# Kernel tuning notes

Hardware: AMD Instinct MI355X
Metric: run time of the kernel (lower is better)

## Reference

```python
import jax, jax.numpy as jnp
import numpy as np

N = 50000      # nodes
E = 800000     # edges (before self-loops)
F_IN = 128
F_OUT = 128
H = 4          # heads
SLOPE = 0.2    # LeakyReLU negative slope (PyG GATConv default)


def setup_inputs() -> dict:
    key = jax.random.key(0)
    ks = jax.random.split(key, 8)
    x = jax.random.normal(ks[0], (N, F_IN), dtype=jnp.float32)
    edge_index = jax.random.randint(ks[1], (2, E), 0, N, dtype=jnp.int64)
    W = jax.random.normal(ks[2], (H, F_IN, F_OUT), dtype=jnp.float32) * (1.0 / np.sqrt(F_IN))
    att_src = jax.random.normal(ks[3], (H, F_OUT), dtype=jnp.float32) * (1.0 / np.sqrt(F_OUT))
    att_dst = jax.random.normal(ks[4], (H, F_OUT), dtype=jnp.float32) * (1.0 / np.sqrt(F_OUT))
    bias = jnp.zeros((H, F_OUT), dtype=jnp.float32)
    W_out = jax.random.normal(ks[5], (H * F_OUT, F_OUT), dtype=jnp.float32) * (1.0 / np.sqrt(H * F_OUT))
    b_out = jnp.zeros((F_OUT,), dtype=jnp.float32)
    return {"x": x, "edge_index": edge_index, "W": W, "att_src": att_src,
            "att_dst": att_dst, "bias": bias, "W_out": W_out, "b_out": b_out}


def _gat_head(x, src, dst, W_h, a_src, a_dst, b_h):
    # x: [N, F_in]; src/dst: [E'] edge endpoints (messages flow src -> dst)
    xW = x @ W_h                                   # [N, F_out]
    alpha_s = xW @ a_src                           # [N]
    alpha_d = xW @ a_dst                           # [N]
    logits = alpha_s[src] + alpha_d[dst]           # [E']
    logits = jnp.where(logits > 0, logits, SLOPE * logits)  # leaky_relu
    # segment softmax over edges grouped by destination node
    seg_max = jax.ops.segment_max(logits, dst, num_segments=N)  # [N]
    e = jnp.exp(logits - seg_max[dst])             # [E']
    denom = jax.ops.segment_sum(e, dst, num_segments=N)         # [N]
    alpha = e / denom[dst]                         # [E']
    # weighted scatter-aggregate of source features to destinations
    out = jax.ops.segment_sum(alpha[:, None] * xW[src], dst, num_segments=N)  # [N, F_out]
    return out + b_h


def reference(x, edge_index, W, att_src, att_dst, bias, W_out, b_out):
    # add self-loops (PyG GATConv default)
    loops = jnp.arange(N, dtype=edge_index.dtype)
    src = jnp.concatenate([edge_index[0], loops])
    dst = jnp.concatenate([edge_index[1], loops])
    heads = [_gat_head(x, src, dst, W[h], att_src[h], att_dst[h], bias[h]) for h in range(H)]
    h_cat = jnp.concatenate(heads, axis=1)         # [N, H*F_out]
    return jax.nn.relu(h_cat @ W_out + b_out)      # [N, F_out]
```

## Files before the change

kernel.cpp:

```cpp
#include <hip/hip_runtime.h>
#include <hip/hip_bf16.h>

constexpr int NN = 50000;
constexpr int EE = 800000;
constexpr float SLOPE = 0.2f;
constexpr int NPAD = 50176;
constexpr int CAP = 64;
constexpr int ZE = NN * CAP;

typedef __bf16 bf16x8 __attribute__((ext_vector_type(8)));
typedef __bf16 bf16x4 __attribute__((ext_vector_type(4)));
typedef float f32x4 __attribute__((ext_vector_type(4)));
typedef float f32x2 __attribute__((ext_vector_type(2)));

__device__ __forceinline__ int edge_at(const int* e32, const long long* e64, int use64, long i) {
    return use64 ? (int)e64[i] : e32[i];
}

__device__ __forceinline__ f32x2 bfpair(unsigned u) {
    f32x2 r;
    r.x = __uint_as_float(u << 16);
    r.y = __uint_as_float(u & 0xffff0000u);
    return r;
}

__global__ void k_prec(const float* __restrict__ W, const float* __restrict__ Wout,
                       const float* __restrict__ att_s, const float* __restrict__ att_d,
                       const float* __restrict__ bias, const float* __restrict__ bout,
                       const long long* e64, int* flag, int* cnt,
                       __bf16* __restrict__ Bfrag, float* __restrict__ wsv, float* __restrict__ wdv,
                       float* __restrict__ cvec, uint4* __restrict__ ew) {
    int b = blockIdx.x, t = threadIdx.x;
    if (b < 512) {
        int h = b >> 7, k = b & 127;
        float acc = 0.f;
        for (int j = 0; j < 128; j++) {
            float w = W[((size_t)(h * 128 + k)) * 128 + j];
            acc += w * Wout[((size_t)(h * 128 + j)) * 128 + t];
        }
        int K = h * 128 + k;
        int k0i = K >> 5, kb = (K >> 3) & 3, jj = K & 7;
        int ni = t >> 4, lr = t & 15;
        Bfrag[(((size_t)k0i * 8 + ni) * 64 + kb * 16 + lr) * 8 + jj] = (__bf16)acc;
    } else if (b == 512) {
        float acc = bout[t];
        for (int j = 0; j < 512; j++) acc += bias[j] * Wout[(size_t)j * 128 + t];
        cvec[t] = acc;
        if (t == 0) ew[ZE] = make_uint4(0u, 0u, 0u, 0u);
    } else if (b < 517) {
        int h = b - 513;
        float as = 0.f, ad = 0.f;
        for (int j = 0; j < 128; j++) {
            float w = W[((size_t)(h * 128 + t)) * 128 + j];
            as += w * att_s[h * 128 + j];
            ad += w * att_d[h * 128 + j];
        }
        wsv[h * 128 + t] = as;
        wdv[h * 128 + t] = ad;
    } else {
        int i = (b - 517) * 128 + t;
        if (i < NN) cnt[i] = 0;
        if (b == 517 && t < 64) {
            long long v = e64[t];
            bool ok = (v >= 0) && (v < (long long)NN);
            unsigned long long m = __ballot(ok);
            if (t == 0) *flag = (m == 0xFFFFFFFFFFFFFFFFull) ? 1 : 0;
        }
    }
}

__global__ __launch_bounds__(256) void k_prep(const float* __restrict__ x, const float* __restrict__ wsv,
                                              const float* __restrict__ wdv, __bf16* __restrict__ xb,
                                              float* __restrict__ as_, float* __restrict__ ad_) {
    int n = blockIdx.x * blockDim.x + threadIdx.x;
    if (n >= NN) return;
    const float4* xr = (const float4*)(x + (size_t)n * 128);
    __bf16* xo = xb + (size_t)n * 128;
    float s[4] = {0, 0, 0, 0}, d[4] = {0, 0, 0, 0};
    for (int q = 0; q < 32; q += 2) {
        float4 v0 = xr[q], v1 = xr[q + 1];
        bf16x8 o;
        o[0] = (__bf16)v0.x; o[1] = (__bf16)v0.y; o[2] = (__bf16)v0.z; o[3] = (__bf16)v0.w;
        o[4] = (__bf16)v1.x; o[5] = (__bf16)v1.y; o[6] = (__bf16)v1.z; o[7] = (__bf16)v1.w;
        *(bf16x8*)(xo + q * 4) = o;
        #pragma unroll
        for (int h = 0; h < 4; h++) {
            float4 a0 = ((const float4*)(wsv + h * 128))[q];
            float4 a1 = ((const float4*)(wsv + h * 128))[q + 1];
            float4 b0 = ((const float4*)(wdv + h * 128))[q];
            float4 b1 = ((const float4*)(wdv + h * 128))[q + 1];
            s[h] += v0.x * a0.x + v0.y * a0.y + v0.z * a0.z + v0.w * a0.w
                  + v1.x * a1.x + v1.y * a1.y + v1.z * a1.z + v1.w * a1.w;
            d[h] += v0.x * b0.x + v0.y * b0.y + v0.z * b0.z + v0.w * b0.w
                  + v1.x * b1.x + v1.y * b1.y + v1.z * b1.z + v1.w * b1.w;
        }
    }
    #pragma unroll
    for (int h = 0; h < 4; h++) { as_[n * 4 + h] = s[h]; ad_[n * 4 + h] = d[h]; }
}

__global__ __launch_bounds__(256) void k_scatterB(const int* e32, const long long* e64, const int* flag,
                                                  const float* __restrict__ as_, const float* __restrict__ ad_,
                                                  int* cnt, uint4* __restrict__ ew) {
    long i0 = ((long)blockIdx.x * blockDim.x + threadIdx.x) * 2;
    if (i0 >= (long)EE + NN) return;
    int use64 = *flag;
    int s[2], d[2];
    #pragma unroll
    for (int j = 0; j < 2; j++) {
        long i = i0 + j;
        if (i < EE) { s[j] = edge_at(e32, e64, use64, i); d[j] = edge_at(e32, e64, use64, (long)EE + i); }
        else        { s[j] = (int)(i - EE); d[j] = s[j]; }
    }
    float4 av[2], bv[2];
    #pragma unroll
    for (int j = 0; j < 2; j++) av[j] = *(const float4*)(as_ + (size_t)s[j] * 4);
    #pragma unroll
    for (int j = 0; j < 2; j++) bv[j] = *(const float4*)(ad_ + (size_t)d[j] * 4);
    int pos[2];
    #pragma unroll
    for (int j = 0; j < 2; j++) pos[j] = d[j] * CAP + atomicAdd(&cnt[d[j]], 1);
    #pragma unroll
    for (int j = 0; j < 2; j++) {
        float l0 = av[j].x + bv[j].x; l0 = l0 > 0.f ? l0 : SLOPE * l0;
        float l1 = av[j].y + bv[j].y; l1 = l1 > 0.f ? l1 : SLOPE * l1;
        float l2 = av[j].z + bv[j].z; l2 = l2 > 0.f ? l2 : SLOPE * l2;
        float l3 = av[j].w + bv[j].w; l3 = l3 > 0.f ? l3 : SLOPE * l3;
        bf16x4 w;
        w[0] = (__bf16)__expf(l0);
        w[1] = (__bf16)__expf(l1);
        w[2] = (__bf16)__expf(l2);
        w[3] = (__bf16)__expf(l3);
        uint2 wp = *(uint2*)&w;
        ew[pos[j]] = make_uint4((unsigned)s[j], wp.x, wp.y, 0u);
    }
}

__global__ __launch_bounds__(256) void k_agg2(const int* __restrict__ cnt, const uint4* __restrict__ ew,
                                              const __bf16* __restrict__ xb, __bf16* __restrict__ agg) {
    int lane = threadIdx.x & 63;
    int half = lane >> 5;
    int sub = lane & 31;
    int n = blockIdx.x * 8 + ((threadIdx.x >> 6) << 1) + half;
    int deg = cnt[n];
    int beg = n * CAP;
    int last = beg + deg - 1;
    int dmax = max(deg, __shfl_xor(deg, 32));
    int nit = (dmax + 3) >> 2;
    f32x2 a01[4] = {}, a23[4] = {};
    f32x2 dn01 = {0.f, 0.f}, dn23 = {0.f, 0.f};
    size_t fo = 4 * (size_t)sub;
    int e = beg;
    for (int it = 0; it < nit; ++it, e += 4) {
        int i0 = (e     <= last) ? e     : ZE;
        int i1 = (e + 1 <= last) ? e + 1 : ZE;
        int i2 = (e + 2 <= last) ? e + 2 : ZE;
        int i3 = (e + 3 <= last) ? e + 3 : ZE;
        uint4 r0 = ew[i0], r1 = ew[i1], r2 = ew[i2], r3 = ew[i3];
        uint2 x0 = *(const uint2*)(xb + (size_t)r0.x * 128 + fo);
        uint2 x1 = *(const uint2*)(xb + (size_t)r1.x * 128 + fo);
        uint2 x2 = *(const uint2*)(xb + (size_t)r2.x * 128 + fo);
        uint2 x3 = *(const uint2*)(xb + (size_t)r3.x * 128 + fo);
#define ACC4(R, XR) { \
        f32x2 w01 = bfpair(R.y), w23 = bfpair(R.z); \
        f32x2 x01 = bfpair(XR.x), x23 = bfpair(XR.y); \
        f32x2 q0 = {w01.x, w01.x}, q1 = {w01.y, w01.y}; \
        f32x2 q2 = {w23.x, w23.x}, q3 = {w23.y, w23.y}; \
        a01[0] += q0 * x01; a23[0] += q0 * x23; \
        a01[1] += q1 * x01; a23[1] += q1 * x23; \
        a01[2] += q2 * x01; a23[2] += q2 * x23; \
        a01[3] += q3 * x01; a23[3] += q3 * x23; \
        dn01 += w01; dn23 += w23; }
        ACC4(r0, x0) ACC4(r1, x1) ACC4(r2, x2) ACC4(r3, x3)
#undef ACC4
    }
    float inv[4];
    inv[0] = 1.f / dn01.x; inv[1] = 1.f / dn01.y;
    inv[2] = 1.f / dn23.x; inv[3] = 1.f / dn23.y;
    __bf16* ar = agg + (size_t)n * 512 + fo;
    #pragma unroll
    for (int h = 0; h < 4; h++) {
        bf16x4 o;
        o[0] = (__bf16)(a01[h].x * inv[h]); o[1] = (__bf16)(a01[h].y * inv[h]);
        o[2] = (__bf16)(a23[h].x * inv[h]); o[3] = (__bf16)(a23[h].y * inv[h]);
        *(bf16x4*)(ar + h * 128) = o;
    }
}

__global__ __launch_bounds__(128) void k_gemmF(const __bf16* __restrict__ agg, const __bf16* __restrict__ Bfrag,
                                               const float* __restrict__ cvec, float* __restrict__ y) {
    int t = threadIdx.x;
    int wv = t >> 6, l = t & 63;
    int lr = l & 15, kb = l >> 4;
    int row0 = blockIdx.x * 64 + wv * 32;
    f32x4 acc[2][8] = {};
    for (int k0i = 0; k0i < 16; k0i++) {
        int kk = k0i * 32 + kb * 8;
        bf16x8 a[2];
        #pragma unroll
        for (int mi = 0; mi < 2; mi++) {
            int g = row0 + mi * 16 + lr;
            a[mi] = *(const bf16x8*)(agg + (size_t)g * 512 + kk);
        }
        #pragma unroll
        for (int ni = 0; ni < 8; ni++) {
            bf16x8 b = *(const bf16x8*)(Bfrag + (((size_t)k0i * 8 + ni) * 64 + l) * 8);
            #pragma unroll
            for (int mi = 0; mi < 2; mi++)
                acc[mi][ni] = __builtin_amdgcn_mfma_f32_16x16x32_bf16(a[mi], b, acc[mi][ni], 0, 0, 0);
        }
    }
    #pragma unroll
    for (int mi = 0; mi < 2; mi++) {
        #pragma unroll
        for (int ni = 0; ni < 8; ni++) {
            int c = ni * 16 + lr;
            float cv = cvec[c];
            #pragma unroll
            for (int r = 0; r < 4; r++) {
                int g = row0 + mi * 16 + kb * 4 + r;
                if (g < NN) y[(size_t)g * 128 + c] = fmaxf(acc[mi][ni][r] + cv, 0.f);
            }
        }
    }
}

extern "C" void kernel_launch(void* const* d_in, const int* in_sizes, int n_in,
                              void* d_out, int out_size, void* d_ws, size_t ws_size,
                              hipStream_t stream) {
    const float* x     = (const float*)d_in[0];
    const void*  ei    = d_in[1];
    const float* W     = (const float*)d_in[2];
    const float* att_s = (const float*)d_in[3];
    const float* att_d = (const float*)d_in[4];
    const float* bias  = (const float*)d_in[5];
    const float* Wout  = (const float*)d_in[6];
    const float* bout  = (const float*)d_in[7];
    float* y = (float*)d_out;

    const int* e32 = (const int*)ei;
    const long long* e64 = (const long long*)ei;

    char* ws = (char*)d_ws;
    size_t off = 0;
    auto alloc = [&](size_t bytes) -> void* {
        void* p = ws + off;
        off = (off + bytes + 255) & ~(size_t)255;
        return p;
    };
    __bf16* agg   = (__bf16*)alloc((size_t)NPAD * 512 * 2);
    __bf16* xb    = (__bf16*)alloc((size_t)NN * 128 * 2);
    uint4* ew     = (uint4*)alloc(((size_t)NN * CAP + 1) * 16);
    float* as_    = (float*)alloc((size_t)NN * 4 * 4);
    float* ad_    = (float*)alloc((size_t)NN * 4 * 4);
    __bf16* Bfrag = (__bf16*)alloc((size_t)512 * 128 * 2);
    float* wsv    = (float*)alloc(4 * 128 * 4);
    float* wdv    = (float*)alloc(4 * 128 * 4);
    float* cvec   = (float*)alloc(128 * 4);
    int* cnt      = (int*)alloc((size_t)NN * 4);
    int* flag     = (int*)alloc(4);

    int precBlocks = 517 + (NN + 127) / 128;
    k_prec<<<precBlocks, 128, 0, stream>>>(W, Wout, att_s, att_d, bias, bout,
                                           e64, flag, cnt, Bfrag, wsv, wdv, cvec, ew);
    k_prep<<<(NN + 255) / 256, 256, 0, stream>>>(x, wsv, wdv, xb, as_, ad_);
    k_scatterB<<<((EE + NN) / 2 + 255) / 256, 256, 0, stream>>>(e32, e64, flag, as_, ad_, cnt, ew);
    k_agg2<<<NN / 8, 256, 0, stream>>>(cnt, ew, xb, agg);
    k_gemmF<<<NPAD / 64, 128, 0, stream>>>(agg, Bfrag, cvec, y);
}
```

Measured before the change: 154.1 us.

## Write edge records in edge order and scatter only 4-byte indices into buckets

The scatter kernel now writes each 16-byte edge record (source plus bf16 weights) coalesced at its edge index, and only scatters a 4-byte edge id into the per-destination bucket with the atomic slot. The aggregation kernel adds an indirection (bucket to edge id to record) and unrolls to 8 edges per iteration for more memory parallelism. This cuts scattered 16-byte writes in exchange for an extra dependent gather level in aggregation, and one edge per thread in the scatter kernel.

Result: slower. 164.7 us (+6.9%).

```diff
diff --git a/kernel.cpp b/kernel.cpp
--- a/kernel.cpp
+++ b/kernel.cpp
@@ -6,7 +6,8 @@
 constexpr float SLOPE = 0.2f;
 constexpr int NPAD = 50176;
 constexpr int CAP = 64;
-constexpr int ZE = NN * CAP;
+constexpr int ZSLOT = NN * CAP;
+constexpr int ZEID = EE + NN;
 
 typedef __bf16 bf16x8 __attribute__((ext_vector_type(8)));
 typedef __bf16 bf16x4 __attribute__((ext_vector_type(4)));
@@ -29,7 +30,7 @@
                        const float* __restrict__ bias, const float* __restrict__ bout,
                        const long long* e64, int* flag, int* cnt,
                        __bf16* __restrict__ Bfrag, float* __restrict__ wsv, float* __restrict__ wdv,
-                       float* __restrict__ cvec, uint4* __restrict__ ew) {
+                       float* __restrict__ cvec, uint4* __restrict__ ewL, int* __restrict__ colv) {
     int b = blockIdx.x, t = threadIdx.x;
     if (b < 512) {
         int h = b >> 7, k = b & 127;
@@ -46,7 +47,10 @@
         float acc = bout[t];
         for (int j = 0; j < 512; j++) acc += bias[j] * Wout[(size_t)j * 128 + t];
         cvec[t] = acc;
-        if (t == 0) ew[ZE] = make_uint4(0u, 0u, 0u, 0u);
+        if (t == 0) {
+            ewL[ZEID] = make_uint4(0u, 0u, 0u, 0u);
+            colv[ZSLOT] = ZEID;
+        }
     } else if (b < 517) {
         int h = b - 513;
         float as = 0.f, ad = 0.f;
@@ -101,42 +105,32 @@
 
 __global__ __launch_bounds__(256) void k_scatterB(const int* e32, const long long* e64, const int* flag,
                                                   const float* __restrict__ as_, const float* __restrict__ ad_,
-                                                  int* cnt, uint4* __restrict__ ew) {
-    long i0 = ((long)blockIdx.x * blockDim.x + threadIdx.x) * 2;
-    if (i0 >= (long)EE + NN) return;
+                                                  int* cnt, int* __restrict__ colv, uint4* __restrict__ ewL) {
+    long i = (long)blockIdx.x * blockDim.x + threadIdx.x;
+    if (i >= (long)EE + NN) return;
     int use64 = *flag;
-    int s[2], d[2];
-    #pragma unroll
-    for (int j = 0; j < 2; j++) {
-        long i = i0 + j;
-        if (i < EE) { s[j] = edge_at(e32, e64, use64, i); d[j] = edge_at(e32, e64, use64, (long)EE + i); }
-        else        { s[j] = (int)(i - EE); d[j] = s[j]; }
-    }
-    float4 av[2], bv[2];
-    #pragma unroll
-    for (int j = 0; j < 2; j++) av[j] = *(const float4*)(as_ + (size_t)s[j] * 4);
-    #pragma unroll
-    for (int j = 0; j < 2; j++) bv[j] = *(const float4*)(ad_ + (size_t)d[j] * 4);
-    int pos[2];
-    #pragma unroll
-    for (int j = 0; j < 2; j++) pos[j] = d[j] * CAP + atomicAdd(&cnt[d[j]], 1);
-    #pragma unroll
-    for (int j = 0; j < 2; j++) {
-        float l0 = av[j].x + bv[j].x; l0 = l0 > 0.f ? l0 : SLOPE * l0;
-        float l1 = av[j].y + bv[j].y; l1 = l1 > 0.f ? l1 : SLOPE * l1;
-        float l2 = av[j].z + bv[j].z; l2 = l2 > 0.f ? l2 : SLOPE * l2;
-        float l3 = av[j].w + bv[j].w; l3 = l3 > 0.f ? l3 : SLOPE * l3;
-        bf16x4 w;
-        w[0] = (__bf16)__expf(l0);
-        w[1] = (__bf16)__expf(l1);
-        w[2] = (__bf16)__expf(l2);
-        w[3] = (__bf16)__expf(l3);
-        uint2 wp = *(uint2*)&w;
-        ew[pos[j]] = make_uint4((unsigned)s[j], wp.x, wp.y, 0u);
-    }
-}
-
-__global__ __launch_bounds__(256) void k_agg2(const int* __restrict__ cnt, const uint4* __restrict__ ew,
+    int s, d;
+    if (i < EE) { s = edge_at(e32, e64, use64, i); d = edge_at(e32, e64, use64, (long)EE + i); }
+    else        { s = (int)(i - EE); d = s; }
+    float4 av = *(const float4*)(as_ + (size_t)s * 4);
+    float4 bv = *(const float4*)(ad_ + (size_t)d * 4);
+    float l0 = av.x + bv.x; l0 = l0 > 0.f ? l0 : SLOPE * l0;
+    float l1 = av.y + bv.y; l1 = l1 > 0.f ? l1 : SLOPE * l1;
+    float l2 = av.z + bv.z; l2 = l2 > 0.f ? l2 : SLOPE * l2;
+    float l3 = av.w + bv.w; l3 = l3 > 0.f ? l3 : SLOPE * l3;
+    bf16x4 w;
+    w[0] = (__bf16)__expf(l0);
+    w[1] = (__bf16)__expf(l1);
+    w[2] = (__bf16)__expf(l2);
+    w[3] = (__bf16)__expf(l3);
+    uint2 wp = *(uint2*)&w;
+    ewL[i] = make_uint4((unsigned)s, wp.x, wp.y, 0u);
+    int pos = d * CAP + atomicAdd(&cnt[d], 1);
+    colv[pos] = (int)i;
+}
+
+__global__ __launch_bounds__(256) void k_agg2(const int* __restrict__ cnt, const int* __restrict__ colv,
+                                              const uint4* __restrict__ ewL,
                                               const __bf16* __restrict__ xb, __bf16* __restrict__ agg) {
     int lane = threadIdx.x & 63;
     int half = lane >> 5;
@@ -146,22 +140,33 @@
     int beg = n * CAP;
     int last = beg + deg - 1;
     int dmax = max(deg, __shfl_xor(deg, 32));
-    int nit = (dmax + 3) >> 2;
+    int nit = (dmax + 7) >> 3;
     f32x2 a01[4] = {}, a23[4] = {};
     f32x2 dn01 = {0.f, 0.f}, dn23 = {0.f, 0.f};
     size_t fo = 4 * (size_t)sub;
     int e = beg;
-    for (int it = 0; it < nit; ++it, e += 4) {
-        int i0 = (e     <= last) ? e     : ZE;
-        int i1 = (e + 1 <= last) ? e + 1 : ZE;
-        int i2 = (e + 2 <= last) ? e + 2 : ZE;
-        int i3 = (e + 3 <= last) ? e + 3 : ZE;
-        uint4 r0 = ew[i0], r1 = ew[i1], r2 = ew[i2], r3 = ew[i3];
+    for (int it = 0; it < nit; ++it, e += 8) {
+        int i0 = (e     <= last) ? e     : ZSLOT;
+        int i1 = (e + 1 <= last) ? e + 1 : ZSLOT;
+        int i2 = (e + 2 <= last) ? e + 2 : ZSLOT;
+        int i3 = (e + 3 <= last) ? e + 3 : ZSLOT;
+        int i4 = (e + 4 <= last) ? e + 4 : ZSLOT;
+        int i5 = (e + 5 <= last) ? e + 5 : ZSLOT;
+        int i6 = (e + 6 <= last) ? e + 6 : ZSLOT;
+        int i7 = (e + 7 <= last) ? e + 7 : ZSLOT;
+        int d0 = colv[i0], d1 = colv[i1], d2 = colv[i2], d3 = colv[i3];
+        int d4 = colv[i4], d5 = colv[i5], d6 = colv[i6], d7 = colv[i7];
+        uint4 r0 = ewL[d0], r1 = ewL[d1], r2 = ewL[d2], r3 = ewL[d3];
+        uint4 r4 = ewL[d4], r5 = ewL[d5], r6 = ewL[d6], r7 = ewL[d7];
         uint2 x0 = *(const uint2*)(xb + (size_t)r0.x * 128 + fo);
         uint2 x1 = *(const uint2*)(xb + (size_t)r1.x * 128 + fo);
         uint2 x2 = *(const uint2*)(xb + (size_t)r2.x * 128 + fo);
         uint2 x3 = *(const uint2*)(xb + (size_t)r3.x * 128 + fo);
-#define ACC4(R, XR) { \
+        uint2 x4 = *(const uint2*)(xb + (size_t)r4.x * 128 + fo);
+        uint2 x5 = *(const uint2*)(xb + (size_t)r5.x * 128 + fo);
+        uint2 x6 = *(const uint2*)(xb + (size_t)r6.x * 128 + fo);
+        uint2 x7 = *(const uint2*)(xb + (size_t)r7.x * 128 + fo);
+#define ACCP(R, XR) { \
         f32x2 w01 = bfpair(R.y), w23 = bfpair(R.z); \
         f32x2 x01 = bfpair(XR.x), x23 = bfpair(XR.y); \
         f32x2 q0 = {w01.x, w01.x}, q1 = {w01.y, w01.y}; \
@@ -171,8 +176,9 @@
         a01[2] += q2 * x01; a23[2] += q2 * x23; \
         a01[3] += q3 * x01; a23[3] += q3 * x23; \
         dn01 += w01; dn23 += w23; }
-        ACC4(r0, x0) ACC4(r1, x1) ACC4(r2, x2) ACC4(r3, x3)
-#undef ACC4
+        ACCP(r0, x0) ACCP(r1, x1) ACCP(r2, x2) ACCP(r3, x3)
+        ACCP(r4, x4) ACCP(r5, x5) ACCP(r6, x6) ACCP(r7, x7)
+#undef ACCP
     }
     float inv[4];
     inv[0] = 1.f / dn01.x; inv[1] = 1.f / dn01.y;
@@ -250,7 +256,8 @@
     };
     __bf16* agg   = (__bf16*)alloc((size_t)NPAD * 512 * 2);
     __bf16* xb    = (__bf16*)alloc((size_t)NN * 128 * 2);
-    uint4* ew     = (uint4*)alloc(((size_t)NN * CAP + 1) * 16);
+    uint4* ewL    = (uint4*)alloc((size_t)(EE + NN + 1) * 16);
+    int* colv     = (int*)alloc(((size_t)NN * CAP + 1) * 4);
     float* as_    = (float*)alloc((size_t)NN * 4 * 4);
     float* ad_    = (float*)alloc((size_t)NN * 4 * 4);
     __bf16* Bfrag = (__bf16*)alloc((size_t)512 * 128 * 2);
@@ -262,9 +269,9 @@
 
     int precBlocks = 517 + (NN + 127) / 128;
     k_prec<<<precBlocks, 128, 0, stream>>>(W, Wout, att_s, att_d, bias, bout,
-                                           e64, flag, cnt, Bfrag, wsv, wdv, cvec, ew);
+                                           e64, flag, cnt, Bfrag, wsv, wdv, cvec, ewL, colv);
     k_prep<<<(NN + 255) / 256, 256, 0, stream>>>(x, wsv, wdv, xb, as_, ad_);
-    k_scatterB<<<((EE + NN) / 2 + 255) / 256, 256, 0, stream>>>(e32, e64, flag, as_, ad_, cnt, ew);
-    k_agg2<<<NN / 8, 256, 0, stream>>>(cnt, ew, xb, agg);
+    k_scatterB<<<(EE + NN + 255) / 256, 256, 0, stream>>>(e32, e64, flag, as_, ad_, cnt, colv, ewL);
+    k_agg2<<<NN / 8, 256, 0, stream>>>(cnt, colv, ewL, xb, agg);
     k_gemmF<<<NPAD / 64, 128, 0, stream>>>(agg, Bfrag, cvec, y);
 }
```

## Fuse neighbor aggregation with output projection GEMM via shared memory tile

Applied to the files above, without the earlier changes.

The aggregation kernel now writes each block's 16 aggregated node rows into an LDS tile. The block then runs the bf16 MFMA projection to the 128 outputs directly, with bias and ReLU, and the separate GEMM kernel is removed. This eliminates the global write and read of the 50000x512 bf16 intermediate and one launch. In exchange, every block reloads the full projection weight fragments from cache, and there is a block-wide barrier between the gather and GEMM phases.

New measurement: 135.6 us. 1.14x faster.

```diff
diff --git a/kernel.cpp b/kernel.cpp
--- a/kernel.cpp
+++ b/kernel.cpp
@@ -4,9 +4,9 @@
 constexpr int NN = 50000;
 constexpr int EE = 800000;
 constexpr float SLOPE = 0.2f;
-constexpr int NPAD = 50176;
 constexpr int CAP = 64;
 constexpr int ZE = NN * CAP;
+constexpr int LDP = 520;
 
 typedef __bf16 bf16x8 __attribute__((ext_vector_type(8)));
 typedef __bf16 bf16x4 __attribute__((ext_vector_type(4)));
@@ -136,91 +136,86 @@
     }
 }
 
-__global__ __launch_bounds__(256) void k_agg2(const int* __restrict__ cnt, const uint4* __restrict__ ew,
-                                              const __bf16* __restrict__ xb, __bf16* __restrict__ agg) {
-    int lane = threadIdx.x & 63;
+__global__ __launch_bounds__(256) void k_aggF(const int* __restrict__ cnt, const uint4* __restrict__ ew,
+                                              const __bf16* __restrict__ xb, const __bf16* __restrict__ Bfrag,
+                                              const float* __restrict__ cvec, float* __restrict__ y) {
+    __shared__ __bf16 aggL[16 * LDP];
+    int t = threadIdx.x;
+    int lane = t & 63;
     int half = lane >> 5;
     int sub = lane & 31;
-    int n = blockIdx.x * 8 + ((threadIdx.x >> 6) << 1) + half;
-    int deg = cnt[n];
-    int beg = n * CAP;
-    int last = beg + deg - 1;
-    int dmax = max(deg, __shfl_xor(deg, 32));
-    int nit = (dmax + 3) >> 2;
-    f32x2 a01[4] = {}, a23[4] = {};
-    f32x2 dn01 = {0.f, 0.f}, dn23 = {0.f, 0.f};
+    int hw = ((t >> 6) << 1) + half;
     size_t fo = 4 * (size_t)sub;
-    int e = beg;
-    for (int it = 0; it < nit; ++it, e += 4) {
-        int i0 = (e     <= last) ? e     : ZE;
-        int i1 = (e + 1 <= last) ? e + 1 : ZE;
-        int i2 = (e + 2 <= last) ? e + 2 : ZE;
-        int i3 = (e + 3 <= last) ? e + 3 : ZE;
-        uint4 r0 = ew[i0], r1 = ew[i1], r2 = ew[i2], r3 = ew[i3];
-        uint2 x0 = *(const uint2*)(xb + (size_t)r0.x * 128 + fo);
-        uint2 x1 = *(const uint2*)(xb + (size_t)r1.x * 128 + fo);
-        uint2 x2 = *(const uint2*)(xb + (size_t)r2.x * 128 + fo);
-        uint2 x3 = *(const uint2*)(xb + (size_t)r3.x * 128 + fo);
-#define ACC4(R, XR) { \
-        f32x2 w01 = bfpair(R.y), w23 = bfpair(R.z); \
-        f32x2 x01 = bfpair(XR.x), x23 = bfpair(XR.y); \
-        f32x2 q0 = {w01.x, w01.x}, q1 = {w01.y, w01.y}; \
-        f32x2 q2 = {w23.x, w23.x}, q3 = {w23.y, w23.y}; \
-        a01[0] += q0 * x01; a23[0] += q0 * x23; \
-        a01[1] += q1 * x01; a23[1] += q1 * x23; \
-        a01[2] += q2 * x01; a23[2] += q2 * x23; \
-        a01[3] += q3 * x01; a23[3] += q3 * x23; \
-        dn01 += w01; dn23 += w23; }
-        ACC4(r0, x0) ACC4(r1, x1) ACC4(r2, x2) ACC4(r3, x3)
-#undef ACC4
-    }
-    float inv[4];
-    inv[0] = 1.f / dn01.x; inv[1] = 1.f / dn01.y;
-    inv[2] = 1.f / dn23.x; inv[3] = 1.f / dn23.y;
-    __bf16* ar = agg + (size_t)n * 512 + fo;
-    #pragma unroll
-    for (int h = 0; h < 4; h++) {
-        bf16x4 o;
-        o[0] = (__bf16)(a01[h].x * inv[h]); o[1] = (__bf16)(a01[h].y * inv[h]);
-        o[2] = (__bf16)(a23[h].x * inv[h]); o[3] = (__bf16)(a23[h].y * inv[h]);
-        *(bf16x4*)(ar + h * 128) = o;
-    }
-}
-
-__global__ __launch_bounds__(128) void k_gemmF(const __bf16* __restrict__ agg, const __bf16* __restrict__ Bfrag,
-                                               const float* __restrict__ cvec, float* __restrict__ y) {
-    int t = threadIdx.x;
-    int wv = t >> 6, l = t & 63;
-    int lr = l & 15, kb = l >> 4;
-    int row0 = blockIdx.x * 64 + wv * 32;
-    f32x4 acc[2][8] = {};
+
+    #pragma unroll
+    for (int r = 0; r < 2; r++) {
+        int nl = r * 8 + hw;
+        int n = blockIdx.x * 16 + nl;
+        int deg = cnt[n];
+        int beg = n * CAP;
+        int last = beg + deg - 1;
+        int dmax = max(deg, __shfl_xor(deg, 32));
+        int nit = (dmax + 3) >> 2;
+        f32x2 a01[4] = {}, a23[4] = {};
+        f32x2 dn01 = {0.f, 0.f}, dn23 = {0.f, 0.f};
+        int e = beg;
+        for (int it = 0; it < nit; ++it, e += 4) {
+            int i0 = (e     <= last) ? e     : ZE;
+            int i1 = (e + 1 <= last) ? e + 1 : ZE;
+            int i2 = (e + 2 <= last) ? e + 2 : ZE;
+            int i3 = (e + 3 <= last) ? e + 3 : ZE;
+            uint4 r0 = ew[i0], r1 = ew[i1], r2 = ew[i2], r3 = ew[i3];
+            uint2 x0 = *(const uint2*)(xb + (size_t)r0.x * 128 + fo);
+            uint2 x1 = *(const uint2*)(xb + (size_t)r1.x * 128 + fo);
+            uint2 x2 = *(const uint2*)(xb + (size_t)r2.x * 128 + fo);
+            uint2 x3 = *(const uint2*)(xb + (size_t)r3.x * 128 + fo);
+#define ACCP(R, XR) { \
+            f32x2 w01 = bfpair(R.y), w23 = bfpair(R.z); \
+            f32x2 x01 = bfpair(XR.x), x23 = bfpair(XR.y); \
+            f32x2 q0 = {w01.x, w01.x}, q1 = {w01.y, w01.y}; \
+            f32x2 q2 = {w23.x, w23.x}, q3 = {w23.y, w23.y}; \
+            a01[0] += q0 * x01; a23[0] += q0 * x23; \
+            a01[1] += q1 * x01; a23[1] += q1 * x23; \
+            a01[2] += q2 * x01; a23[2] += q2 * x23; \
+            a01[3] += q3 * x01; a23[3] += q3 * x23; \
+            dn01 += w01; dn23 += w23; }
+            ACCP(r0, x0) ACCP(r1, x1) ACCP(r2, x2) ACCP(r3, x3)
+#undef ACCP
+        }
+        float inv[4];
+        inv[0] = 1.f / dn01.x; inv[1] = 1.f / dn01.y;
+        inv[2] = 1.f / dn23.x; inv[3] = 1.f / dn23.y;
+        __bf16* ar = aggL + nl * LDP + fo;
+        #pragma unroll
+        for (int h = 0; h < 4; h++) {
+            bf16x4 o;
+            o[0] = (__bf16)(a01[h].x * inv[h]); o[1] = (__bf16)(a01[h].y * inv[h]);
+            o[2] = (__bf16)(a23[h].x * inv[h]); o[3] = (__bf16)(a23[h].y * inv[h]);
+            *(bf16x4*)(ar + h * 128) = o;
+        }
+    }
+    __syncthreads();
+
+    int w = t >> 6;
+    int lr = lane & 15, kb = lane >> 4;
+    f32x4 acc[2] = {};
     for (int k0i = 0; k0i < 16; k0i++) {
-        int kk = k0i * 32 + kb * 8;
-        bf16x8 a[2];
-        #pragma unroll
-        for (int mi = 0; mi < 2; mi++) {
-            int g = row0 + mi * 16 + lr;
-            a[mi] = *(const bf16x8*)(agg + (size_t)g * 512 + kk);
-        }
-        #pragma unroll
-        for (int ni = 0; ni < 8; ni++) {
-            bf16x8 b = *(const bf16x8*)(Bfrag + (((size_t)k0i * 8 + ni) * 64 + l) * 8);
-            #pragma unroll
-            for (int mi = 0; mi < 2; mi++)
-                acc[mi][ni] = __builtin_amdgcn_mfma_f32_16x16x32_bf16(a[mi], b, acc[mi][ni], 0, 0, 0);
-        }
-    }
-    #pragma unroll
-    for (int mi = 0; mi < 2; mi++) {
-        #pragma unroll
-        for (int ni = 0; ni < 8; ni++) {
-            int c = ni * 16 + lr;
-            float cv = cvec[c];
-            #pragma unroll
-            for (int r = 0; r < 4; r++) {
-                int g = row0 + mi * 16 + kb * 4 + r;
-                if (g < NN) y[(size_t)g * 128 + c] = fmaxf(acc[mi][ni][r] + cv, 0.f);
-            }
+        bf16x8 a = *(const bf16x8*)(aggL + lr * LDP + k0i * 32 + kb * 8);
+        #pragma unroll
+        for (int ni = 0; ni < 2; ni++) {
+            int ni_g = w * 2 + ni;
+            bf16x8 b = *(const bf16x8*)(Bfrag + (((size_t)k0i * 8 + ni_g) * 64 + lane) * 8);
+            acc[ni] = __builtin_amdgcn_mfma_f32_16x16x32_bf16(a, b, acc[ni], 0, 0, 0);
+        }
+    }
+    int row0 = blockIdx.x * 16 + kb * 4;
+    #pragma unroll
+    for (int ni = 0; ni < 2; ni++) {
+        int c = (w * 2 + ni) * 16 + lr;
+        float cv = cvec[c];
+        #pragma unroll
+        for (int r = 0; r < 4; r++) {
+            y[(size_t)(row0 + r) * 128 + c] = fmaxf(acc[ni][r] + cv, 0.f);
         }
     }
 }
@@ -248,7 +243,6 @@
         off = (off + bytes + 255) & ~(size_t)255;
         return p;
     };
-    __bf16* agg   = (__bf16*)alloc((size_t)NPAD * 512 * 2);
     __bf16* xb    = (__bf16*)alloc((size_t)NN * 128 * 2);
     uint4* ew     = (uint4*)alloc(((size_t)NN * CAP + 1) * 16);
     float* as_    = (float*)alloc((size_t)NN * 4 * 4);
@@ -265,6 +259,5 @@
                                            e64, flag, cnt, Bfrag, wsv, wdv, cvec, ew);
     k_prep<<<(NN + 255) / 256, 256, 0, stream>>>(x, wsv, wdv, xb, as_, ad_);
     k_scatterB<<<((EE + NN) / 2 + 255) / 256, 256, 0, stream>>>(e32, e64, flag, as_, ad_, cnt, ew);
-    k_agg2<<<NN / 8, 256, 0, stream>>>(cnt, ew, xb, agg);
-    k_gemmF<<<NPAD / 64, 128, 0, stream>>>(agg, Bfrag, cvec, y);
-}
+    k_aggF<<<NN / 16, 256, 0, stream>>>(cnt, ew, xb, Bfrag, cvec, y);
+}
```
